# Performance work log

Measured on AMD Instinct MI355X. Metric: run time of the kernel, lower is better.

Reference implementation:

```python
import jax, jax.numpy as jnp
from jax import lax
import numpy as np

B, Hd, Wd, Cd, D, HID = 64, 16, 16, 32, 64, 256


def setup_inputs() -> dict:
    key = jax.random.key(0)
    k0, k1, k2, k3, k4 = jax.random.split(key, 5)
    std = 1.0 / np.sqrt(HID)
    x = jax.random.normal(k0, (B, Hd, Wd, Cd, D), dtype=jnp.float32)
    # Linear weights stored as (in, out); torch Linear computes x @ W.T + b
    W_in = jax.random.uniform(k1, (D, HID), jnp.float32, -std, std)
    b_in = jax.random.uniform(k2, (HID,), jnp.float32, -std, std)
    W_h = jax.random.uniform(k3, (3 * HID, HID), jnp.float32, -std, std)
    b_h = jax.random.uniform(k4, (HID,), jnp.float32, -std, std)
    return {"x": x, "W_in": W_in, "b_in": b_in, "W_h": W_h, "b_h": b_h}


def reference(x, W_in, b_in, W_h, b_h):
    b, h, w, c, d = x.shape
    H = W_in.shape[1]
    # Precompute input projection for all positions (same math, hoisted out of loops)
    xp = jnp.einsum('bhwcd,dk->bhwck', x, W_in) + b_in  # (b,h,w,c,H)
    xp = jnp.transpose(xp, (1, 2, 3, 0, 4))             # (h,w,c,b,H)
    # Split hidden_layer weight by which previous-state block it multiplies:
    # cat(h_prev1, h_prev2, h_prev3) @ W_h = h1@W1 + h2@W2 + h3@W3
    W1, W2, W3 = W_h[:H], W_h[H:2 * H], W_h[2 * H:]

    def scan_k(h_k, inp):
        xp_k, h_up, h_left = inp  # each (b,H)
        hid = jnp.tanh(xp_k + h_up @ W1 + h_left @ W2 + h_k @ W3 + b_h)
        return hid, hid

    def scan_j(h_left_col, inp):
        xp_j, h_up_col = inp  # (c,b,H)
        zero = jnp.zeros((b, H), xp_j.dtype)
        _, h_col = lax.scan(scan_k, zero, (xp_j, h_up_col, h_left_col))
        return h_col, h_col  # (c,b,H)

    def scan_i(h_up_plane, xp_i):
        zero_col = jnp.zeros((c, b, H), xp_i.dtype)
        _, plane = lax.scan(scan_j, zero_col, (xp_i, h_up_plane))
        return plane, plane  # (w,c,b,H)

    zero_plane = jnp.zeros((w, c, b, H), x.dtype)
    _, hidden = lax.scan(scan_i, zero_plane, xp)  # (h,w,c,b,H)
    return jnp.transpose(hidden, (3, 0, 1, 2, 4))  # (b,h,w,c,H)
```

## Files before the change

### kernel.cpp

```cpp
#include <hip/hip_runtime.h>


typedef _Float16 f16x8 __attribute__((ext_vector_type(8)));
typedef float f32x4 __attribute__((ext_vector_type(4)));

#define OUT_BSTRIDE 2097152
#define X_BSTRIDE   524288
#define SLOT_BYTES  32768
#define FLAGS_OFF   1048576
#define RING3_OFF   2097152
#define RING3_BYTES ((size_t)8192 * SLOT_BYTES)
#define SMEM_BYTES  106496
#define FB_PITCH    260

__device__ __forceinline__ void bar_raw() {
  asm volatile("" ::: "memory");
  __builtin_amdgcn_s_barrier();
  asm volatile("" ::: "memory");
}
__device__ __forceinline__ void bar_lgkm() {
  asm volatile("s_waitcnt lgkmcnt(0)" ::: "memory");
  __builtin_amdgcn_sched_barrier(0);
  bar_raw();
}
__device__ __forceinline__ void bar_vm() {
  asm volatile("s_waitcnt vmcnt(0)" ::: "memory");
  __builtin_amdgcn_sched_barrier(0);
  bar_raw();
}

__device__ __forceinline__ void store_wt16(void* p, f16x8 v) {
  asm volatile("global_store_dwordx4 %0, %1, off sc0 sc1" :: "v"(p), "v"(v) : "memory");
}

__device__ __forceinline__ void wait_flag(const unsigned int* f) {
  while (__hip_atomic_load(f, __ATOMIC_RELAXED, __HIP_MEMORY_SCOPE_SYSTEM) == 0u)
    __builtin_amdgcn_s_sleep(2);
  asm volatile("" ::: "memory");
}

__device__ __forceinline__ f16x8 conv8f16(const f32x4& a, const f32x4& b) {
  f16x8 r;
  r[0] = (_Float16)a[0]; r[1] = (_Float16)a[1];
  r[2] = (_Float16)a[2]; r[3] = (_Float16)a[3];
  r[4] = (_Float16)b[0]; r[5] = (_Float16)b[1];
  r[6] = (_Float16)b[2]; r[7] = (_Float16)b[3];
  return r;
}

#define GL_AS1(p) ((const __attribute__((address_space(1))) unsigned int*)(p))
#define LDS_AS3(p) ((__attribute__((address_space(3))) unsigned int*)(p))

__device__ __forceinline__ void gll_copy4(const unsigned char* slot, unsigned char* buf,
                                          int w, int lane) {
#pragma unroll
  for (int it = 0; it < 4; ++it) {
    const unsigned char* g = slot + it * 8192 + w * 1024 + lane * 16;
    unsigned char* l = buf + it * 8192 + w * 1024;
    __builtin_amdgcn_global_load_lds(GL_AS1(g), LDS_AS3(l), 16, 0, 0);
  }
}

template<int KS, int PITCH>
__device__ __forceinline__ void mm1(f32x4 (&acc)[4][2], const unsigned char* smem,
                                    const _Float16* __restrict__ wt,
                                    int ncol0, int l15, int l4, int swz) {
#pragma unroll
  for (int kk = 0; kk < KS / 32; ++kk) {
    const int k0 = kk * 32 + l4 * 8;
    f16x8 ah[4], bh[2];
#pragma unroll
    for (int mi = 0; mi < 4; ++mi) {
      int byte = (mi * 16 + l15) * PITCH + ((k0 * 2) ^ swz);
      ah[mi] = *(const f16x8*)(smem + byte);
    }
#pragma unroll
    for (int ni = 0; ni < 2; ++ni) {
      int n = ncol0 + ni * 16 + l15;
      bh[ni] = *(const f16x8*)(wt + n * KS + k0);
    }
#pragma unroll
    for (int mi = 0; mi < 4; ++mi)
#pragma unroll
      for (int ni = 0; ni < 2; ++ni)
        acc[mi][ni] = __builtin_amdgcn_mfma_f32_16x16x32_f16(ah[mi], bh[ni], acc[mi][ni], 0, 0, 0);
  }
}

template<int KS, int PITCH>
__device__ __forceinline__ void mm1r(f32x4 (&acc)[4][2], const unsigned char* smem,
                                     const f16x8 (&bh)[KS / 32][2],
                                     int l15, int l4, int swz) {
#pragma unroll
  for (int kk = 0; kk < KS / 32; ++kk) {
    const int k0 = kk * 32 + l4 * 8;
    f16x8 ah[4];
#pragma unroll
    for (int mi = 0; mi < 4; ++mi) {
      int byte = (mi * 16 + l15) * PITCH + ((k0 * 2) ^ swz);
      ah[mi] = *(const f16x8*)(smem + byte);
    }
#pragma unroll
    for (int mi = 0; mi < 4; ++mi)
#pragma unroll
      for (int ni = 0; ni < 2; ++ni)
        acc[mi][ni] = __builtin_amdgcn_mfma_f32_16x16x32_f16(ah[mi], bh[kk][ni], acc[mi][ni], 0, 0, 0);
  }
}

template<int BPR, int ITERS, int PITCH>
__device__ __forceinline__ void stage_f16(const float* __restrict__ src, int rstride,
                                          unsigned char* buf, int t) {
#pragma unroll
  for (int it = 0; it < ITERS; ++it) {
    int c = t + it * 512;
    int row = c / BPR, bk = c % BPR;
    const float* p = src + row * rstride + bk * 8;
    f32x4 v0 = *(const f32x4*)p;
    f32x4 v1 = *(const f32x4*)(p + 4);
    f16x8 h8 = conv8f16(v0, v1);
    int byte = row * PITCH + ((bk * 16) ^ ((row & 7) << 4));
    *(f16x8*)(buf + byte) = h8;
  }
}

__global__ void mdrnn_prep(const float* __restrict__ W_in, const float* __restrict__ b_in,
                           const float* __restrict__ W_h, const float* __restrict__ b_h,
                           unsigned char* __restrict__ ws) {
  int t = blockIdx.x * 256 + threadIdx.x;
  float* bias = (float*)ws;
  _Float16* win = (_Float16*)(ws + 1024);
  _Float16* wh0 = win + 16384;

  if (t < 256) bias[t] = b_in[t] + b_h[t];
  if (t < 8192)
    __hip_atomic_store((unsigned int*)(ws + FLAGS_OFF) + t, 0u,
                       __ATOMIC_RELAXED, __HIP_MEMORY_SCOPE_SYSTEM);
  if (t < 16384) {
    int n = t >> 6, k = t & 63;
    win[t] = (_Float16)W_in[k * 256 + n];
  }
  if (t < 196608) {
    int m = t >> 16;
    int r = t & 65535;
    int n = r >> 8, k = r & 255;
    (wh0 + m * 65536)[r] = (_Float16)W_h[(m * 256 + k) * 256 + n];
  }
}

__global__ __launch_bounds__(512, 2)
void mdrnn_persist(const float* __restrict__ x, const unsigned char* __restrict__ ws,
                   unsigned char* __restrict__ ring, unsigned int* __restrict__ flags,
                   float* __restrict__ out) {
  const int bx = blockIdx.x;
  const int i = bx >> 4, j = bx & 15;

  __shared__ __align__(16) unsigned char smem[SMEM_BYTES];
  unsigned char* P = smem;
  unsigned char* R = smem + 32768;
  unsigned char* L = smem + 65536;
  unsigned char* X = smem + 98304;
  float* fbuf = (float*)(smem + 32768);

  const int t = threadIdx.x;
  const int lane = t & 63;
  const int w = t >> 6;
  const int l15 = lane & 15, l4 = lane >> 4;
  const int swz = (lane & 7) << 4;
  const int ncol0 = w * 32;

  const float* bias = (const float*)ws;
  const _Float16* win = (const _Float16*)(ws + 1024);
  const _Float16* w1 = win + 16384;
  const _Float16* w2 = w1 + 65536;
  const _Float16* w3 = w2 + 65536;

  const int cell2 = bx;
  const unsigned int* upF   = flags + (size_t)(cell2 - 16) * 32;
  const unsigned int* leftF = flags + (size_t)(cell2 - 1) * 32;
  unsigned int* myF = flags + (size_t)cell2 * 32;
  const bool has_cons = (i < 15) || (j < 15);

  f16x8 wbI[2][2], wb3[8][2];
#pragma unroll
  for (int kk = 0; kk < 2; ++kk)
#pragma unroll
    for (int ni = 0; ni < 2; ++ni) {
      int n = ncol0 + ni * 16 + l15;
      wbI[kk][ni] = *(const f16x8*)(win + n * 64 + kk * 32 + l4 * 8);
    }
#pragma unroll
  for (int kk = 0; kk < 8; ++kk)
#pragma unroll
    for (int ni = 0; ni < 2; ++ni) {
      int n = ncol0 + ni * 16 + l15;
      wb3[kk][ni] = *(const f16x8*)(w3 + n * 256 + kk * 32 + l4 * 8);
    }
  float bias2[2];
#pragma unroll
  for (int ni = 0; ni < 2; ++ni) bias2[ni] = bias[ncol0 + ni * 16 + l15];

  const int xrow = t >> 3, xck = t & 7;
  const float* xbase = x + (size_t)xrow * X_BSTRIDE + (size_t)cell2 * 32 * 64 + xck * 8;
  f32x4 xr0 = __builtin_nontemporal_load((const f32x4*)xbase);
  f32x4 xr1 = __builtin_nontemporal_load((const f32x4*)(xbase + 4));

  f32x4 vo0[4], vo1[4];

  for (int k = 0; k < 32; ++k) {
    const int cell3 = cell2 * 32 + k;

    {
      f16x8 h8 = conv8f16(xr0, xr1);
      int byte = xrow * 128 + ((xck * 16) ^ ((xrow & 7) << 4));
      *(f16x8*)(X + byte) = h8;
    }
    bar_lgkm();

    f32x4 acc[4][2];
#pragma unroll
    for (int mi = 0; mi < 4; ++mi)
#pragma unroll
      for (int ni = 0; ni < 2; ++ni)
        acc[mi][ni] = f32x4{0.f, 0.f, 0.f, 0.f};

    if (k > 0) {
      float* oc = out + (size_t)(cell3 - 1) * 256;
#pragma unroll
      for (int it = 0; it < 4; ++it) {
        int c = t + it * 512;
        int row = c >> 5, ck = c & 31;
        float* op = oc + (size_t)row * OUT_BSTRIDE + ck * 8;
        __builtin_nontemporal_store(vo0[it], (f32x4*)op);
        __builtin_nontemporal_store(vo1[it], (f32x4*)(op + 4));
      }
    }

    mm1r<64, 128>(acc, X, wbI, l15, l4, swz);
    if (k > 0) mm1r<256, 512>(acc, P, wb3, l15, l4, swz);

    if (i > 0 && t == 0)  wait_flag(upF + k);
    if (j > 0 && t == 64) wait_flag(leftF + k);
    bar_raw();
    __builtin_amdgcn_sched_barrier(0);
    if (i > 0) gll_copy4(ring + (size_t)((cell2 - 16) * 32 + k) * SLOT_BYTES, R, w, lane);
    if (j > 0) gll_copy4(ring + (size_t)((cell2 - 1) * 32 + k) * SLOT_BYTES, L, w, lane);
    {
      int kn = (k < 31) ? k + 1 : 31;
      xr0 = __builtin_nontemporal_load((const f32x4*)(xbase + kn * 64));
      xr1 = __builtin_nontemporal_load((const f32x4*)(xbase + kn * 64 + 4));
    }
    __builtin_amdgcn_sched_barrier(0);

    if (i > 0) {
      if (j > 0) { asm volatile("s_waitcnt vmcnt(6)" ::: "memory"); }
      else       { asm volatile("s_waitcnt vmcnt(2)" ::: "memory"); }
      __builtin_amdgcn_sched_barrier(0);
      bar_raw();
      mm1<256, 512>(acc, R, w1, ncol0, l15, l4, swz);
    }
    if (j > 0) {
      asm volatile("s_waitcnt vmcnt(2)" ::: "memory");
      __builtin_amdgcn_sched_barrier(0);
      bar_raw();
      mm1<256, 512>(acc, L, w2, ncol0, l15, l4, swz);
    }

    bar_raw();
#pragma unroll
    for (int mi = 0; mi < 4; ++mi)
#pragma unroll
      for (int ni = 0; ni < 2; ++ni) {
        float bv = bias2[ni];
        int col = ncol0 + ni * 16 + l15;
#pragma unroll
        for (int r = 0; r < 4; ++r) {
          int row = mi * 16 + l4 * 4 + r;
          float v = acc[mi][ni][r] + bv;
          float e = __expf(2.f * v);
          fbuf[row * FB_PITCH + col] = 1.f - 2.f / (e + 1.f);
        }
      }
    bar_lgkm();

    unsigned char* slotW = ring + (size_t)cell3 * SLOT_BYTES;
#pragma unroll
    for (int it = 0; it < 4; ++it) {
      int c = t + it * 512;
      int row = c >> 5, ck = c & 31;
      const float* p = fbuf + row * FB_PITCH + ck * 8;
      f32x4 v0 = *(const f32x4*)p;
      f32x4 v1 = *(const f32x4*)(p + 4);
      vo0[it] = v0;
      vo1[it] = v1;
      f16x8 h8 = conv8f16(v0, v1);
      int byte = row * 512 + ((ck * 16) ^ ((row & 7) << 4));
      *(f16x8*)(P + byte) = h8;
      if (has_cons) store_wt16(slotW + byte, h8);
    }

    bar_vm();
    if (has_cons && t == 0)
      __hip_atomic_store(myF + k, 1u, __ATOMIC_RELAXED, __HIP_MEMORY_SCOPE_SYSTEM);
  }

  {
    float* oc = out + (size_t)(cell2 * 32 + 31) * 256;
#pragma unroll
    for (int it = 0; it < 4; ++it) {
      int c = t + it * 512;
      int row = c >> 5, ck = c & 31;
      float* op = oc + (size_t)row * OUT_BSTRIDE + ck * 8;
      __builtin_nontemporal_store(vo0[it], (f32x4*)op);
      __builtin_nontemporal_store(vo1[it], (f32x4*)(op + 4));
    }
  }
}

__global__ __launch_bounds__(512)
void mdrnn_cell2(int s, const float* __restrict__ x, const unsigned char* __restrict__ ws,
                 float* __restrict__ out) {
  const int bx = blockIdx.x;
  const int i = bx >> 4, j = bx & 15;
  const int kc = s - i - j;
  if (kc < 0 || kc >= 32) return;

  __shared__ __align__(16) unsigned char smem[SMEM_BYTES];
  const int t = threadIdx.x;
  const int lane = t & 63;
  const int w = t >> 6;
  const int l15 = lane & 15, l4 = lane >> 4;
  const int swz = (lane & 7) << 4;
  const int ncol0 = w * 32;
  unsigned char* ABUF = smem;
  unsigned char* XBUF = smem + 32768;
  float* fbuf = (float*)smem;

  const float* bias = (const float*)ws;
  const _Float16* win = (const _Float16*)(ws + 1024);
  const _Float16* w1 = win + 16384;
  const _Float16* w2 = w1 + 65536;
  const _Float16* w3 = w2 + 65536;

  const int cell3 = (i * 16 + j) * 32 + kc;

  f32x4 acc[4][2];
#pragma unroll
  for (int mi = 0; mi < 4; ++mi)
#pragma unroll
    for (int ni = 0; ni < 2; ++ni)
      acc[mi][ni] = f32x4{0.f, 0.f, 0.f, 0.f};

  stage_f16<8, 1, 128>(x + (size_t)cell3 * 64, X_BSTRIDE, XBUF, t);
  bar_lgkm();
  mm1<64, 128>(acc, XBUF, win, ncol0, l15, l4, swz);

  if (j > 0) {
    bar_raw();
    stage_f16<32, 4, 512>(out + (size_t)(cell3 - 32) * 256, OUT_BSTRIDE, ABUF, t);
    bar_lgkm();
    mm1<256, 512>(acc, ABUF, w2, ncol0, l15, l4, swz);
  }
  if (i > 0) {
    bar_raw();
    stage_f16<32, 4, 512>(out + (size_t)(cell3 - 512) * 256, OUT_BSTRIDE, ABUF, t);
    bar_lgkm();
    mm1<256, 512>(acc, ABUF, w1, ncol0, l15, l4, swz);
  }
  if (kc > 0) {
    bar_raw();
    stage_f16<32, 4, 512>(out + (size_t)(cell3 - 1) * 256, OUT_BSTRIDE, ABUF, t);
    bar_lgkm();
    mm1<256, 512>(acc, ABUF, w3, ncol0, l15, l4, swz);
  }

  bar_raw();
#pragma unroll
  for (int mi = 0; mi < 4; ++mi)
#pragma unroll
    for (int ni = 0; ni < 2; ++ni) {
      int col = ncol0 + ni * 16 + l15;
      float bv = bias[col];
#pragma unroll
      for (int r = 0; r < 4; ++r) {
        int row = mi * 16 + l4 * 4 + r;
        float v = acc[mi][ni][r] + bv;
        float e = __expf(2.f * v);
        fbuf[row * FB_PITCH + col] = 1.f - 2.f / (e + 1.f);
      }
    }
  bar_lgkm();
#pragma unroll
  for (int it = 0; it < 4; ++it) {
    int c = t + it * 512;
    int row = c >> 5, ck = c & 31;
    const float* p = fbuf + row * FB_PITCH + ck * 8;
    f32x4 v0 = *(const f32x4*)p;
    f32x4 v1 = *(const f32x4*)(p + 4);
    float* op = out + (size_t)row * OUT_BSTRIDE + (size_t)cell3 * 256 + ck * 8;
    *(f32x4*)op = v0;
    *(f32x4*)(op + 4) = v1;
  }
}

extern "C" void kernel_launch(void* const* d_in, const int* in_sizes, int n_in,
                              void* d_out, int out_size, void* d_ws, size_t ws_size,
                              hipStream_t stream) {
  const float* x    = (const float*)d_in[0];
  const float* W_in = (const float*)d_in[1];
  const float* b_in = (const float*)d_in[2];
  const float* W_h  = (const float*)d_in[3];
  const float* b_h  = (const float*)d_in[4];
  float* out = (float*)d_out;
  unsigned char* ws = (unsigned char*)d_ws;

  mdrnn_prep<<<768, 256, 0, stream>>>(W_in, b_in, W_h, b_h, ws);

  if (ws_size >= (size_t)RING3_OFF + RING3_BYTES) {
    mdrnn_persist<<<256, 512, 0, stream>>>(x, ws, ws + RING3_OFF,
                                           (unsigned int*)(ws + FLAGS_OFF), out);
  } else {
    for (int s = 0; s <= 61; ++s)
      mdrnn_cell2<<<256, 512, 0, stream>>>(s, x, ws, out);
  }
}
```

Before: 911.0 us.

## Split recurrent matmul to overlap ring loads and merge neighbor waits

Splits the self-recurrent (W3) matmul into two K halves and runs the second half after the up/left ring copies are issued, so useful MFMA work hides the global-load latency. The two separate waits and barriers for the up and left neighbor tiles become a single wait and barrier before both matmuls. The tanh is now computed in registers before the barrier that guards the fbuf write rather than after it, which shortens the serialized section. The price is a longer live range for the prefetched weights and a coarser wait, so the up-neighbor matmul can no longer start before the left copy lands.

New measurement: 894.7 us. Within noise of the previous version (-1.8%).

```diff
diff --git a/kernel.cpp b/kernel.cpp
--- a/kernel.cpp
+++ b/kernel.cpp
@@ -87,12 +87,12 @@
   }
 }
 
-template<int KS, int PITCH>
-__device__ __forceinline__ void mm1r(f32x4 (&acc)[4][2], const unsigned char* smem,
-                                     const f16x8 (&bh)[KS / 32][2],
-                                     int l15, int l4, int swz) {
-#pragma unroll
-  for (int kk = 0; kk < KS / 32; ++kk) {
+template<int PITCH, int KK0, int KK1, int NB>
+__device__ __forceinline__ void mm1r_rng(f32x4 (&acc)[4][2], const unsigned char* smem,
+                                         const f16x8 (&bh)[NB][2],
+                                         int l15, int l4, int swz) {
+#pragma unroll
+  for (int kk = KK0; kk < KK1; ++kk) {
     const int k0 = kk * 32 + l4 * 8;
     f16x8 ah[4];
 #pragma unroll
@@ -236,8 +236,8 @@
       }
     }
 
-    mm1r<64, 128>(acc, X, wbI, l15, l4, swz);
-    if (k > 0) mm1r<256, 512>(acc, P, wb3, l15, l4, swz);
+    mm1r_rng<128, 0, 2, 2>(acc, X, wbI, l15, l4, swz);
+    if (k > 0) mm1r_rng<512, 0, 4, 8>(acc, P, wb3, l15, l4, swz);
 
     if (i > 0 && t == 0)  wait_flag(upF + k);
     if (j > 0 && t == 64) wait_flag(leftF + k);
@@ -252,33 +252,39 @@
     }
     __builtin_amdgcn_sched_barrier(0);
 
-    if (i > 0) {
-      if (j > 0) { asm volatile("s_waitcnt vmcnt(6)" ::: "memory"); }
-      else       { asm volatile("s_waitcnt vmcnt(2)" ::: "memory"); }
-      __builtin_amdgcn_sched_barrier(0);
-      bar_raw();
-      mm1<256, 512>(acc, R, w1, ncol0, l15, l4, swz);
-    }
-    if (j > 0) {
+    if (k > 0) mm1r_rng<512, 4, 8, 8>(acc, P, wb3, l15, l4, swz);
+
+    if (i > 0 || j > 0) {
       asm volatile("s_waitcnt vmcnt(2)" ::: "memory");
       __builtin_amdgcn_sched_barrier(0);
       bar_raw();
-      mm1<256, 512>(acc, L, w2, ncol0, l15, l4, swz);
-    }
-
-    bar_raw();
+      if (i > 0) mm1<256, 512>(acc, R, w1, ncol0, l15, l4, swz);
+      if (j > 0) mm1<256, 512>(acc, L, w2, ncol0, l15, l4, swz);
+    }
+
 #pragma unroll
     for (int mi = 0; mi < 4; ++mi)
 #pragma unroll
       for (int ni = 0; ni < 2; ++ni) {
         float bv = bias2[ni];
+#pragma unroll
+        for (int r = 0; r < 4; ++r) {
+          float v = acc[mi][ni][r] + bv;
+          float e = __expf(2.f * v);
+          acc[mi][ni][r] = 1.f - 2.f / (e + 1.f);
+        }
+      }
+
+    bar_raw();
+#pragma unroll
+    for (int mi = 0; mi < 4; ++mi)
+#pragma unroll
+      for (int ni = 0; ni < 2; ++ni) {
         int col = ncol0 + ni * 16 + l15;
 #pragma unroll
         for (int r = 0; r < 4; ++r) {
           int row = mi * 16 + l4 * 4 + r;
-          float v = acc[mi][ni][r] + bv;
-          float e = __expf(2.f * v);
-          fbuf[row * FB_PITCH + col] = 1.f - 2.f / (e + 1.f);
+          fbuf[row * FB_PITCH + col] = acc[mi][ni][r];
         }
       }
     bar_lgkm();
```
